# Optimization experiments

Measured on AMD Instinct MI355X. Metric: run time of the kernel, lower is better.

Reference implementation:

```python
import jax, jax.numpy as jnp
import numpy as np
import math

EPS = 1e-5  # torch LayerNorm default


def entmax15(z):
    # Peters & Martins exact sort-based alpha=1.5 entmax along last axis.
    z = z / 2.0
    z = z - jnp.max(z, axis=-1, keepdims=True)
    zs = -jnp.sort(-z, axis=-1)                      # descending
    K = z.shape[-1]
    rho = jnp.arange(1, K + 1, dtype=z.dtype)
    mean = jnp.cumsum(zs, axis=-1) / rho
    mean_sq = jnp.cumsum(zs * zs, axis=-1) / rho
    ss = rho * (mean_sq - mean * mean)
    delta = jnp.clip((1.0 - ss) / rho, 0.0)
    tau = mean - jnp.sqrt(delta)
    k = jnp.sum(tau <= zs, axis=-1, keepdims=True)   # support size
    tau_star = jnp.take_along_axis(tau, k - 1, axis=-1)
    p = jnp.square(jnp.clip(z - tau_star, 0.0))
    return p


def mish(x):
    return x * jnp.tanh(jax.nn.softplus(x))


def layer_norm(x, g, b):
    mu = jnp.mean(x, axis=-1, keepdims=True)
    var = jnp.var(x, axis=-1, keepdims=True)
    return (x - mu) / jnp.sqrt(var + EPS) * g + b


def setup_inputs() -> dict:
    key = jax.random.key(0)
    D, H, F = 512, 8, 2048
    B, S = 8, 1024
    ks = jax.random.split(key, 16)
    s = 1.0 / math.sqrt(D)
    inp = {
        "x": jax.random.normal(ks[0], (B, S, D), jnp.float32),
        # weights stored [in, out]; y = x @ W + b
        "Wq": jax.random.normal(ks[1], (D, D), jnp.float32) * s,
        "bq": jnp.zeros((D,), jnp.float32),
        "Wk": jax.random.normal(ks[2], (D, D), jnp.float32) * s,
        "bk": jnp.zeros((D,), jnp.float32),
        "Wv": jax.random.normal(ks[3], (D, D), jnp.float32) * s,
        "bv": jnp.zeros((D,), jnp.float32),
        "Wo": jax.random.normal(ks[4], (D, D), jnp.float32) * s,
        "bo": jnp.zeros((D,), jnp.float32),
        "g1": jnp.ones((D,), jnp.float32),
        "be1": jnp.zeros((D,), jnp.float32),
        "W1": jax.random.normal(ks[5], (D, F), jnp.float32) * s,
        "b1": jnp.zeros((F,), jnp.float32),
        "W2": jax.random.normal(ks[6], (F, D), jnp.float32) * (1.0 / math.sqrt(F)),
        "b2": jnp.zeros((D,), jnp.float32),
        "g2": jnp.ones((D,), jnp.float32),
        "be2": jnp.zeros((D,), jnp.float32),
    }
    return inp


def reference(x, Wq, bq, Wk, bk, Wv, bv, Wo, bo, g1, be1, W1, b1, W2, b2, g2, be2):
    B, S, D = x.shape
    H = 8
    hd = D // H
    # multi-head self-attention (z = x)
    q = (x @ Wq + bq).reshape(B, S, H, hd).transpose(0, 2, 1, 3)
    k = (x @ Wk + bk).reshape(B, S, H, hd).transpose(0, 2, 1, 3)
    v = (x @ Wv + bv).reshape(B, S, H, hd).transpose(0, 2, 1, 3)
    scores = jnp.einsum("bhqd,bhkd->bhqk", q, k) / math.sqrt(hd)
    attn = entmax15(scores)
    out = jnp.einsum("bhqk,bhkd->bhqd", attn, v)
    out = out.transpose(0, 2, 1, 3).reshape(B, S, D)
    y = out @ Wo + bo
    x = x + layer_norm(y, g1, be1)
    # feed-forward with Mish
    y = mish(x @ W1 + b1) @ W2 + b2
    x = x + layer_norm(y, g2, be2)
    return x
```

## Files before the change

### kernel.cpp

```cpp
#include <hip/hip_runtime.h>


typedef float f32x4 __attribute__((ext_vector_type(4)));
typedef float f32x2 __attribute__((ext_vector_type(2)));
typedef __bf16 b8 __attribute__((ext_vector_type(8)));

#define DEV static __device__ __forceinline__

DEV unsigned short f2bf(float f) {
  return __builtin_bit_cast(unsigned short, (__bf16)f);
}
DEV float bf2f(unsigned short b) { return __uint_as_float(((unsigned)b) << 16); }

DEV float mishf(float x) {
  if (x > 20.f) return x;
  float e = __expf(x);
  float u = 1.f + e;
  u *= u;
  return x * ((u - 1.f) / (u + 1.f));
}

DEV void async16(const void* g, void* l) {
  __builtin_amdgcn_global_load_lds(
      (const __attribute__((address_space(1))) unsigned int*)g,
      (__attribute__((address_space(3))) unsigned int*)l, 16, 0, 0);
}

DEV int mbcnt64(unsigned long long m) {
  return __builtin_amdgcn_mbcnt_hi((unsigned)(m >> 32),
                                   __builtin_amdgcn_mbcnt_lo((unsigned)m, 0));
}

template <int CTRL>
DEV float dppmov(float x) {
  return __builtin_bit_cast(
      float, __builtin_amdgcn_update_dpp(0, __builtin_bit_cast(int, x), CTRL,
                                         0xF, 0xF, true));
}
DEV float swz16(float x) {
  return __builtin_bit_cast(
      float, __builtin_amdgcn_ds_swizzle(__builtin_bit_cast(int, x), 0x401F));
}
DEV float wave_sum(float x) {
  x += dppmov<0xB1>(x);
  x += dppmov<0x4E>(x);
  x += dppmov<0x141>(x);
  x += dppmov<0x140>(x);
  x += swz16(x);
  x += __shfl_xor(x, 32);
  return x;
}
DEV float wave_max(float x) {
  x = fmaxf(x, dppmov<0xB1>(x));
  x = fmaxf(x, dppmov<0x4E>(x));
  x = fmaxf(x, dppmov<0x141>(x));
  x = fmaxf(x, dppmov<0x140>(x));
  x = fmaxf(x, swz16(x));
  x = fmaxf(x, __shfl_xor(x, 32));
  return x;
}

template <int WM, int WN, int EPI, bool OUTBF>
__global__ __launch_bounds__(256) void gemm_bt(
    const unsigned short* __restrict__ A, const unsigned short* __restrict__ Bt,
    const float* __restrict__ bias, void* __restrict__ Cp,
    int K, int lda, int ldb, int ldc,
    long sA1, long sA2, long sB1, long sB2, long sC1, long sC2,
    int hdiv, float alpha) {
  constexpr int BM = WM * 64, BN = WN * 64;
  constexpr int NA = WM * 2, NB = WN * 2;
  __shared__ unsigned short smA[BM * 64];
  __shared__ unsigned short smB[BN * 64];

  const int tid = threadIdx.x;
  const int lane = tid & 63;
  const int z = blockIdx.z;
  const long zi = z / hdiv, zr = z % hdiv;
  const unsigned short* Ab = A + zi * sA1 + zr * sA2 + (long)blockIdx.x * BM * lda;
  const unsigned short* Bb = Bt + zi * sB1 + zr * sB2 + (long)blockIdx.y * BN * ldb;

  int siA[NA];
  const unsigned short* gA[NA];
#pragma unroll
  for (int q = 0; q < NA; ++q) {
    int si = q * 256 + tid;
    int m = si >> 3, s = si & 7, g = s ^ (m & 7);
    siA[q] = si;
    gA[q] = Ab + (long)m * lda + g * 8;
  }
  int siB[NB];
  const unsigned short* gB[NB];
#pragma unroll
  for (int q = 0; q < NB; ++q) {
    int si = q * 256 + tid;
    int m = si >> 3, s = si & 7, g = s ^ (m & 7);
    siB[q] = si;
    gB[q] = Bb + (long)m * ldb + g * 8;
  }

  const int w = tid >> 6;
  const int wr = w / WN, wc = w % WN;
  const int fm = lane & 15, fg = lane >> 4;

  int aOff[4][2], bOff[4][2];
#pragma unroll
  for (int i = 0; i < 4; ++i)
#pragma unroll
    for (int ks = 0; ks < 2; ++ks) {
      int m = wr * 64 + i * 16 + fm;
      aOff[i][ks] = (m * 8 + ((ks * 4 + fg) ^ (fm & 7))) * 8;
      int n = wc * 64 + i * 16 + fm;
      bOff[i][ks] = (n * 8 + ((ks * 4 + fg) ^ (fm & 7))) * 8;
    }

  f32x4 acc[4][4];
#pragma unroll
  for (int i = 0; i < 4; ++i)
#pragma unroll
    for (int j = 0; j < 4; ++j) acc[i][j] = (f32x4){0.f, 0.f, 0.f, 0.f};

  for (int k0 = 0; k0 < K; k0 += 64) {
    __syncthreads();
#pragma unroll
    for (int q = 0; q < NA; ++q) async16(gA[q] + k0, (void*)&smA[siA[q] * 8]);
#pragma unroll
    for (int q = 0; q < NB; ++q) async16(gB[q] + k0, (void*)&smB[siB[q] * 8]);
    __syncthreads();

#pragma unroll
    for (int ks = 0; ks < 2; ++ks) {
      b8 aF[4], bF[4];
#pragma unroll
      for (int i = 0; i < 4; ++i) aF[i] = *(const b8*)&smA[aOff[i][ks]];
#pragma unroll
      for (int j = 0; j < 4; ++j) bF[j] = *(const b8*)&smB[bOff[j][ks]];
#pragma unroll
      for (int i = 0; i < 4; ++i)
#pragma unroll
        for (int j = 0; j < 4; ++j)
          acc[i][j] = __builtin_amdgcn_mfma_f32_16x16x32_bf16(aF[i], bF[j], acc[i][j], 0, 0, 0);
    }
  }

  const long cbase = zi * sC1 + zr * sC2;
  const int row0 = blockIdx.x * BM + wr * 64 + fg * 4;
  const int col0 = blockIdx.y * BN + wc * 64 + fm;
#pragma unroll
  for (int i = 0; i < 4; ++i) {
#pragma unroll
    for (int j = 0; j < 4; ++j) {
      const int col = col0 + j * 16;
      float bv = (EPI >= 1) ? bias[col] : 0.f;
#pragma unroll
      for (int r = 0; r < 4; ++r) {
        const int row = row0 + i * 16 + r;
        float v = acc[i][j][r] * alpha + bv;
        if (EPI == 2) v = mishf(v);
        const long idx = cbase + (long)row * ldc + col;
        if constexpr (OUTBF)
          ((unsigned short*)Cp)[idx] = f2bf(v);
        else
          ((float*)Cp)[idx] = v;
      }
    }
  }
}

__global__ __launch_bounds__(256) void gemm_scores(
    const unsigned short* __restrict__ QKV, unsigned short* __restrict__ P) {
  __shared__ unsigned short smB[128 * 64];

  const int tid = threadIdx.x, lane = tid & 63, w = tid >> 6;
  const int wr = w >> 1, wc = w & 1;
  const int fm = lane & 15, fg = lane >> 4;
  const int z = blockIdx.z, b = z >> 3, h = z & 7;
  const long qrow0 = (long)b * 1024 + blockIdx.x * 128;
  const long krow0 = (long)b * 1024 + blockIdx.y * 128;

#pragma unroll
  for (int q = 0; q < 4; ++q) {
    int si = q * 256 + tid;
    int m = si >> 3, s = si & 7, g = s ^ (m & 7);
    async16(QKV + (krow0 + m) * 1536 + 512 + h * 64 + g * 8, (void*)&smB[si * 8]);
  }

  b8 aQ[4][2];
#pragma unroll
  for (int i = 0; i < 4; ++i) {
    const unsigned short* qp =
        QKV + (qrow0 + wr * 64 + i * 16 + fm) * 1536 + h * 64 + fg * 8;
    aQ[i][0] = *(const b8*)qp;
    aQ[i][1] = *(const b8*)(qp + 32);
  }

  __syncthreads();

  f32x4 acc[4][4];
#pragma unroll
  for (int i = 0; i < 4; ++i)
#pragma unroll
    for (int j = 0; j < 4; ++j) acc[i][j] = (f32x4){0.f, 0.f, 0.f, 0.f};

#pragma unroll
  for (int ks = 0; ks < 2; ++ks) {
    b8 bF[4];
#pragma unroll
    for (int j = 0; j < 4; ++j) {
      int n = wc * 64 + j * 16 + fm;
      bF[j] = *(const b8*)&smB[(n * 8 + ((ks * 4 + fg) ^ (fm & 7))) * 8];
    }
#pragma unroll
    for (int i = 0; i < 4; ++i)
#pragma unroll
      for (int j = 0; j < 4; ++j)
        acc[i][j] = __builtin_amdgcn_mfma_f32_16x16x32_bf16(aQ[i][ks], bF[j], acc[i][j], 0, 0, 0);
  }

  unsigned short* Pb = P + (long)z * 1024 * 1024;
  const int row0 = blockIdx.x * 128 + wr * 64 + fg * 4;
  const int col0 = blockIdx.y * 128 + wc * 64 + fm;
#pragma unroll
  for (int i = 0; i < 4; ++i)
#pragma unroll
    for (int j = 0; j < 4; ++j)
#pragma unroll
      for (int r = 0; r < 4; ++r)
        Pb[(long)(row0 + i * 16 + r) * 1024 + col0 + j * 16] =
            f2bf(acc[i][j][r] * 0.0625f);
}

__global__ __launch_bounds__(256) void gemm_pv(
    const unsigned short* __restrict__ P, const unsigned short* __restrict__ Vt,
    const float* __restrict__ Tau, unsigned short* __restrict__ attn) {
  __shared__ unsigned short smA[256 * 64];
  __shared__ unsigned short smB[64 * 64];

  const int tid = threadIdx.x, lane = tid & 63, w = tid >> 6;
  const int fm = lane & 15, fg = lane >> 4;
  const int z = blockIdx.z;
  const long SS = 1024L * 1024L;
  const unsigned short* Ab = P + (long)z * SS + (long)blockIdx.x * 256 * 1024;
  const unsigned short* Bb = Vt + (long)z * 64 * 1024;
  const float* Tb = Tau + (long)z * 1024 + blockIdx.x * 256;

  int siA[8];
  const unsigned short* gA[8];
  float tq[8];
#pragma unroll
  for (int q = 0; q < 8; ++q) {
    int si = q * 256 + tid;
    int m = si >> 3, s = si & 7, g = s ^ (m & 7);
    siA[q] = si;
    gA[q] = Ab + (long)m * 1024 + g * 8;
    tq[q] = Tb[m];
  }
  int siB[2];
  const unsigned short* gB[2];
#pragma unroll
  for (int q = 0; q < 2; ++q) {
    int si = q * 256 + tid;
    int m = si >> 3, s = si & 7, g = s ^ (m & 7);
    siB[q] = si;
    gB[q] = Bb + (long)m * 1024 + g * 8;
  }

  int aOff[4][2], bOff[4][2];
#pragma unroll
  for (int i = 0; i < 4; ++i)
#pragma unroll
    for (int ks = 0; ks < 2; ++ks) {
      int m = w * 64 + i * 16 + fm;
      aOff[i][ks] = (m * 8 + ((ks * 4 + fg) ^ (fm & 7))) * 8;
      int n = i * 16 + fm;
      bOff[i][ks] = (n * 8 + ((ks * 4 + fg) ^ (fm & 7))) * 8;
    }

  f32x4 acc[4][4];
#pragma unroll
  for (int i = 0; i < 4; ++i)
#pragma unroll
    for (int j = 0; j < 4; ++j) acc[i][j] = (f32x4){0.f, 0.f, 0.f, 0.f};

  union AB { b8 v; unsigned short u[8]; };
  for (int k0 = 0; k0 < 1024; k0 += 64) {
    __syncthreads();
    AB areg[8];
#pragma unroll
    for (int q = 0; q < 8; ++q) areg[q].v = *(const b8*)(gA[q] + k0);
#pragma unroll
    for (int q = 0; q < 2; ++q) async16(gB[q] + k0, (void*)&smB[siB[q] * 8]);
#pragma unroll
    for (int q = 0; q < 8; ++q) {
      AB o;
#pragma unroll
      for (int e = 0; e < 8; ++e) {
        float h = fmaxf(bf2f(areg[q].u[e]) - tq[q], 0.f);
        o.u[e] = f2bf(h * h);
      }
      *(b8*)&smA[siA[q] * 8] = o.v;
    }
    __syncthreads();

#pragma unroll
    for (int ks = 0; ks < 2; ++ks) {
      b8 aF[4], bF[4];
#pragma unroll
      for (int i = 0; i < 4; ++i) aF[i] = *(const b8*)&smA[aOff[i][ks]];
#pragma unroll
      for (int j = 0; j < 4; ++j) bF[j] = *(const b8*)&smB[bOff[j][ks]];
#pragma unroll
      for (int i = 0; i < 4; ++i)
#pragma unroll
        for (int j = 0; j < 4; ++j)
          acc[i][j] = __builtin_amdgcn_mfma_f32_16x16x32_bf16(aF[i], bF[j], acc[i][j], 0, 0, 0);
    }
  }

  const long cbase = (long)(z >> 3) * 1024 * 512 + (z & 7) * 64;
  const int row0 = blockIdx.x * 256 + w * 64 + fg * 4;
#pragma unroll
  for (int i = 0; i < 4; ++i)
#pragma unroll
    for (int j = 0; j < 4; ++j) {
      const int col = fm + j * 16;
#pragma unroll
      for (int r = 0; r < 4; ++r) {
        const int row = row0 + i * 16 + r;
        attn[cbase + (long)row * 512 + col] = f2bf(acc[i][j][r]);
      }
    }
}

__global__ __launch_bounds__(256) void gemm_ffn1(
    const unsigned short* __restrict__ A, const unsigned short* __restrict__ Bt,
    const float* __restrict__ bias, unsigned short* __restrict__ C) {
  __shared__ unsigned short smA[2 * 128 * 64];
  __shared__ unsigned short smB[2 * 128 * 64];

  const int tid = threadIdx.x;
  const int lane = tid & 63;
  const unsigned short* Ab = A + (long)blockIdx.x * 128 * 512;
  const unsigned short* Bb = Bt + (long)blockIdx.y * 128 * 512;

  int siA[4], siB[4];
  const unsigned short* gA[4];
  const unsigned short* gB[4];
#pragma unroll
  for (int q = 0; q < 4; ++q) {
    int si = q * 256 + tid;
    int m = si >> 3, s = si & 7, g = s ^ (m & 7);
    siA[q] = si;
    siB[q] = si;
    gA[q] = Ab + (long)m * 512 + g * 8;
    gB[q] = Bb + (long)m * 512 + g * 8;
  }

  const int w = tid >> 6;
  const int wr = w >> 1, wc = w & 1;
  const int fm = lane & 15, fg = lane >> 4;

  int aOff[4][2], bOff[4][2];
#pragma unroll
  for (int i = 0; i < 4; ++i)
#pragma unroll
    for (int ks = 0; ks < 2; ++ks) {
      int m = wr * 64 + i * 16 + fm;
      aOff[i][ks] = (m * 8 + ((ks * 4 + fg) ^ (fm & 7))) * 8;
      int n = wc * 64 + i * 16 + fm;
      bOff[i][ks] = (n * 8 + ((ks * 4 + fg) ^ (fm & 7))) * 8;
    }

  f32x4 acc[4][4];
#pragma unroll
  for (int i = 0; i < 4; ++i)
#pragma unroll
    for (int j = 0; j < 4; ++j) acc[i][j] = (f32x4){0.f, 0.f, 0.f, 0.f};

  auto stage = [&](int buf, int k0) {
    unsigned short* dA = smA + buf * (128 * 64);
    unsigned short* dB = smB + buf * (128 * 64);
#pragma unroll
    for (int q = 0; q < 4; ++q) async16(gA[q] + k0, (void*)&dA[siA[q] * 8]);
#pragma unroll
    for (int q = 0; q < 4; ++q) async16(gB[q] + k0, (void*)&dB[siB[q] * 8]);
  };
  auto compute = [&](int buf) {
    const unsigned short* sA = smA + buf * (128 * 64);
    const unsigned short* sB = smB + buf * (128 * 64);
#pragma unroll
    for (int ks = 0; ks < 2; ++ks) {
      b8 aF[4], bF[4];
#pragma unroll
      for (int i = 0; i < 4; ++i) aF[i] = *(const b8*)&sA[aOff[i][ks]];
#pragma unroll
      for (int j = 0; j < 4; ++j) bF[j] = *(const b8*)&sB[bOff[j][ks]];
#pragma unroll
      for (int i = 0; i < 4; ++i)
#pragma unroll
        for (int j = 0; j < 4; ++j)
          acc[i][j] = __builtin_amdgcn_mfma_f32_16x16x32_bf16(aF[i], bF[j], acc[i][j], 0, 0, 0);
    }
  };

  stage(0, 0);
  __syncthreads();
  int cur = 0;
  for (int k0 = 64; k0 < 512; k0 += 64) {
    stage(cur ^ 1, k0);
    compute(cur);
    __syncthreads();
    cur ^= 1;
  }
  compute(cur);

  const int row0 = blockIdx.x * 128 + wr * 64 + fg * 4;
  const int col0 = blockIdx.y * 128 + wc * 64 + fm;
#pragma unroll
  for (int i = 0; i < 4; ++i) {
#pragma unroll
    for (int j = 0; j < 4; ++j) {
      const int col = col0 + j * 16;
      const float bv = bias[col];
#pragma unroll
      for (int r = 0; r < 4; ++r) {
        const int row = row0 + i * 16 + r;
        C[(long)row * 2048 + col] = f2bf(mishf(acc[i][j][r] + bv));
      }
    }
  }
}

template <int NC>
DEV float solve_tau(const f32x2* zc, float tau) {
  int kprev = -1;
  const f32x2 zero2 = (f32x2){0.f, 0.f};
  for (int it = 0; it < 12; ++it) {
    const f32x2 t2 = (f32x2){tau, tau};
    f32x2 s1v = zero2, s2v = zero2;
    int k = 0;
#pragma unroll
    for (int i = 0; i < NC; ++i) {
      f32x2 h = zc[i] - t2;
      k += __popcll(__ballot(h.x > 0.f));
      k += __popcll(__ballot(h.y > 0.f));
      f32x2 hp = __builtin_elementwise_max(h, zero2);
      s1v += hp;
      s2v += hp * hp;
    }
    float s1 = wave_sum(s1v.x + s1v.y);
    float s2 = wave_sum(s2v.x + s2v.y);
    if (k == kprev) break;
    kprev = k;
    float kf = (float)k;
    float disc = fmaxf(fmaf(s1, s1, -kf * (s2 - 1.f)), 0.f);
    tau += (s1 - __builtin_sqrtf(disc)) / kf;
  }
  return tau;
}

DEV float solve_tau_lds(const float* cw, int nch, int lane, float tau) {
  int kprev = -1;
  const f32x2 zero2 = (f32x2){0.f, 0.f};
  for (int it = 0; it < 12; ++it) {
    const f32x2 t2 = (f32x2){tau, tau};
    f32x2 s1v = zero2, s2v = zero2;
    int k = 0;
    for (int c = 0; c < nch; ++c) {
      f32x2 h = *(const f32x2*)&cw[c * 128 + lane * 2] - t2;
      k += __popcll(__ballot(h.x > 0.f));
      k += __popcll(__ballot(h.y > 0.f));
      f32x2 hp = __builtin_elementwise_max(h, zero2);
      s1v += hp;
      s2v += hp * hp;
    }
    float s1 = wave_sum(s1v.x + s1v.y);
    float s2 = wave_sum(s2v.x + s2v.y);
    if (k == kprev) break;
    kprev = k;
    float kf = (float)k;
    float disc = fmaxf(fmaf(s1, s1, -kf * (s2 - 1.f)), 0.f);
    tau += (s1 - __builtin_sqrtf(disc)) / kf;
  }
  return tau;
}

__global__ __launch_bounds__(256) void entmax_tau(const unsigned short* __restrict__ P,
                                                  float* __restrict__ T) {
  const int tid = threadIdx.x, lane = tid & 63, wv = tid >> 6;
  const long row = (long)blockIdx.x * 4 + wv;
  const unsigned short* p = P + row * 1024;
  __shared__ float cand[4][1024];

  union { uint4 v; unsigned short u[8]; } a, b;
  a.v = *(const uint4*)(p + lane * 16);
  b.v = *(const uint4*)(p + lane * 16 + 8);
  f32x2 zp[8];
#pragma unroll
  for (int i = 0; i < 4; ++i) {
    zp[i] = (f32x2){bf2f(a.u[2 * i]), bf2f(a.u[2 * i + 1])};
    zp[4 + i] = (f32x2){bf2f(b.u[2 * i]), bf2f(b.u[2 * i + 1])};
  }

  f32x2 mv = zp[0];
#pragma unroll
  for (int i = 1; i < 8; ++i) mv = __builtin_elementwise_max(mv, zp[i]);
  float m = wave_max(fmaxf(mv.x, mv.y));

  const float thr = m - 1.f;
  float* cw = cand[wv];

  int base = 0;
#pragma unroll
  for (int i = 0; i < 8; ++i) {
    unsigned long long mx = __ballot(zp[i].x > thr);
    if (zp[i].x > thr) cw[base + mbcnt64(mx)] = zp[i].x;
    base += __popcll(mx);
    unsigned long long my = __ballot(zp[i].y > thr);
    if (zp[i].y > thr) cw[base + mbcnt64(my)] = zp[i].y;
    base += __popcll(my);
  }

  const int nch = (base + 127) >> 7;
  for (int i = base + lane; i < nch * 128; i += 64) cw[i] = -1e30f;

  float tau;
  if (nch == 1) {
    f32x2 zc[1];
    zc[0] = *(const f32x2*)&cw[lane * 2];
    tau = solve_tau<1>(zc, thr);
  } else if (nch == 2) {
    f32x2 zc[2];
    zc[0] = *(const f32x2*)&cw[lane * 2];
    zc[1] = *(const f32x2*)&cw[128 + lane * 2];
    tau = solve_tau<2>(zc, thr);
  } else {
    tau = solve_tau_lds(cw, nch, lane, thr);
  }

  if (lane == 0) T[row] = tau;
}

__global__ __launch_bounds__(256) void prep_all(
    const float* __restrict__ x, unsigned short* __restrict__ xb,
    const float* __restrict__ Wq, const float* __restrict__ Wk,
    const float* __restrict__ Wv, const float* __restrict__ Wo,
    const float* __restrict__ W1, const float* __restrict__ W2,
    unsigned short* __restrict__ Wqkvt, unsigned short* __restrict__ Wot,
    unsigned short* __restrict__ W1t, unsigned short* __restrict__ W2t,
    const float* __restrict__ bq, const float* __restrict__ bk,
    const float* __restrict__ bv, float* __restrict__ bqkv) {
  __shared__ float t[32][33];
  const int bid = blockIdx.x, tid = threadIdx.x;

  if (bid < 4096) {
    long i = ((long)bid * 256 + tid) * 4;
    float4 v = *(const float4*)&x[i];
    uint2 pk;
    pk.x = (unsigned)f2bf(v.x) | ((unsigned)f2bf(v.y) << 16);
    pk.y = (unsigned)f2bf(v.z) | ((unsigned)f2bf(v.w) << 16);
    *(uint2*)&xb[i] = pk;
    return;
  }

  const float* in;
  unsigned short* out;
  int ldi, ldo, bx, by;
  if (bid < 5120) {
    int t4 = (bid - 4096) >> 8, local = (bid - 4096) & 255;
    const float* ins[4] = {Wq, Wk, Wv, Wo};
    unsigned short* outs[4] = {Wqkvt, Wqkvt + 512 * 512, Wqkvt + 2 * 512 * 512, Wot};
    in = ins[t4];
    out = outs[t4];
    ldi = 512;
    ldo = 512;
    bx = local & 15;
    by = local >> 4;
  } else if (bid < 6144) {
    int local = bid - 5120;
    in = W1;
    out = W1t;
    ldi = 2048;
    ldo = 512;
    bx = local & 63;
    by = local >> 6;
  } else if (bid < 7168) {
    int local = bid - 6144;
    in = W2;
    out = W2t;
    ldi = 512;
    ldo = 2048;
    bx = local & 15;
    by = local >> 4;
  } else {
    int i = (bid - 7168) * 256 + tid;
    if (i < 512) bqkv[i] = bq[i];
    else if (i < 1024) bqkv[i] = bk[i - 512];
    else if (i < 1536) bqkv[i] = bv[i - 1024];
    return;
  }

  const int tx = tid & 31, ty = tid >> 5;
  const int r0 = by * 32, c0 = bx * 32;
#pragma unroll
  for (int q = 0; q < 4; ++q) {
    int r = ty + q * 8;
    t[r][tx] = in[(long)(r0 + r) * ldi + c0 + tx];
  }
  __syncthreads();
#pragma unroll
  for (int q = 0; q < 4; ++q) {
    int r = ty + q * 8;
    out[(long)(c0 + r) * ldo + r0 + tx] = f2bf(t[tx][r]);
  }
}

__global__ __launch_bounds__(256) void transpose_b2b(const unsigned short* __restrict__ in,
                                                     unsigned short* __restrict__ out,
                                                     int ldi, int ldo, long i1, long i2,
                                                     long o1, long o2, int hdiv) {
  __shared__ unsigned short t[32][33];
  const int z = blockIdx.z;
  in += (long)(z / hdiv) * i1 + (long)(z % hdiv) * i2;
  out += (long)(z / hdiv) * o1 + (long)(z % hdiv) * o2;
  const int tx = threadIdx.x & 31, ty = threadIdx.x >> 5;
  const int r0 = blockIdx.y * 32, c0 = blockIdx.x * 32;
#pragma unroll
  for (int q = 0; q < 4; ++q) {
    int r = ty + q * 8;
    t[r][tx] = in[(long)(r0 + r) * ldi + c0 + tx];
  }
  __syncthreads();
#pragma unroll
  for (int q = 0; q < 4; ++q) {
    int r = ty + q * 8;
    out[(long)(c0 + r) * ldo + r0 + tx] = t[tx][r];
  }
}

template <bool WB, int NS>
__global__ __launch_bounds__(256) void ln_res(const float* __restrict__ xin,
                                              const float* __restrict__ y, long ystr,
                                              const float* __restrict__ ybias,
                                              const float* __restrict__ g,
                                              const float* __restrict__ be,
                                              float* __restrict__ xo,
                                              unsigned short* __restrict__ xob) {
  const int row = blockIdx.x, tid = threadIdx.x, lane = tid & 63, wv = tid >> 6;
  const long base = (long)row * 512 + tid * 2;
  const int c = tid * 2;
  float2 v = *(const float2*)&y[base];
#pragma unroll
  for (int j = 1; j < NS; ++j) {
    float2 u = *(const float2*)&y[base + j * ystr];
    v.x += u.x;
    v.y += u.y;
  }
  v.x += ybias[c];
  v.y += ybias[c + 1];
  float s1 = wave_sum(v.x + v.y);
  float s2 = wave_sum(v.x * v.x + v.y * v.y);
  __shared__ float red[4][2];
  if (lane == 0) {
    red[wv][0] = s1;
    red[wv][1] = s2;
  }
  __syncthreads();
  s1 = red[0][0] + red[1][0] + red[2][0] + red[3][0];
  s2 = red[0][1] + red[1][1] + red[2][1] + red[3][1];
  const float mu = s1 * (1.f / 512.f);
  const float rstd = rsqrtf(s2 * (1.f / 512.f) - mu * mu + 1e-5f);
  float2 xv = *(const float2*)&xin[base];
  float o0 = xv.x + (v.x - mu) * rstd * g[c] + be[c];
  float o1 = xv.y + (v.y - mu) * rstd * g[c + 1] + be[c + 1];
  float2 ov;
  ov.x = o0;
  ov.y = o1;
  *(float2*)&xo[base] = ov;
  if constexpr (WB) {
    unsigned pk = (unsigned)f2bf(o0) | ((unsigned)f2bf(o1) << 16);
    *(unsigned*)&xob[base] = pk;
  }
}

extern "C" void kernel_launch(void* const* d_in, const int* in_sizes, int n_in,
                              void* d_out, int out_size, void* d_ws, size_t ws_size,
                              hipStream_t stream) {
  const int B = 8, S = 1024, D = 512, H = 8, F = 2048;
  const int BS = B * S;
  const int N3 = 3 * D;

  const float* x = (const float*)d_in[0];
  const float* Wq = (const float*)d_in[1];
  const float* bq = (const float*)d_in[2];
  const float* Wk = (const float*)d_in[3];
  const float* bk = (const float*)d_in[4];
  const float* Wv = (const float*)d_in[5];
  const float* bv = (const float*)d_in[6];
  const float* Wo = (const float*)d_in[7];
  const float* bo = (const float*)d_in[8];
  const float* g1 = (const float*)d_in[9];
  const float* be1 = (const float*)d_in[10];
  const float* W1 = (const float*)d_in[11];
  const float* b1 = (const float*)d_in[12];
  const float* W2 = (const float*)d_in[13];
  const float* b2 = (const float*)d_in[14];
  const float* g2 = (const float*)d_in[15];
  const float* be2 = (const float*)d_in[16];
  float* out = (float*)d_out;

  char* w = (char*)d_ws;
  size_t off = 0;
  auto alloc = [&](size_t bytes) -> void* {
    void* p = w + off;
    off += bytes;
    off = (off + 255) & ~(size_t)255;
    return p;
  };

  unsigned short* xb = (unsigned short*)alloc((size_t)BS * D * 2);
  unsigned short* Wqkvt = (unsigned short*)alloc((size_t)N3 * D * 2);
  unsigned short* Wot = (unsigned short*)alloc((size_t)D * D * 2);
  unsigned short* W1t = (unsigned short*)alloc((size_t)F * D * 2);
  unsigned short* W2t = (unsigned short*)alloc((size_t)D * F * 2);
  float* bqkv = (float*)alloc((size_t)N3 * 4);
  unsigned short* QKVb = (unsigned short*)alloc((size_t)BS * N3 * 2);
  unsigned short* Vt = (unsigned short*)alloc((size_t)BS * D * 2);
  unsigned short* attn = (unsigned short*)alloc((size_t)BS * D * 2);
  unsigned short* P = (unsigned short*)alloc((size_t)B * H * S * S * 2);
  float* Tau = (float*)alloc((size_t)B * H * S * 4);
  float* x1 = (float*)alloc((size_t)BS * D * 4);
  unsigned short* hb = (unsigned short*)alloc((size_t)BS * F * 2);
  unsigned short* x1b = xb;
  float* yp = (float*)P;
  const long PSTR = (long)BS * D;

  prep_all<<<7174, 256, 0, stream>>>(x, xb, Wq, Wk, Wv, Wo, W1, W2,
                                     Wqkvt, Wot, W1t, W2t, bq, bk, bv, bqkv);

  gemm_bt<2, 2, 1, true><<<dim3(BS / 128, N3 / 128, 1), 256, 0, stream>>>(
      xb, Wqkvt, bqkv, QKVb, D, D, D, N3, 0, 0, 0, 0, 0, 0, 1, 1.f);

  transpose_b2b<<<dim3(2, 32, 64), 256, 0, stream>>>(
      QKVb + 1024, Vt, N3, S, (long)S * N3, 64, (long)8 * 64 * S, (long)64 * S, 8);

  gemm_scores<<<dim3(S / 128, S / 128, B * H), 256, 0, stream>>>(QKVb, P);

  entmax_tau<<<(B * H * S) / 4, 256, 0, stream>>>(P, Tau);

  gemm_pv<<<dim3(S / 256, 1, B * H), 256, 0, stream>>>(P, Vt, Tau, attn);

  gemm_bt<2, 2, 0, false><<<dim3(BS / 128, D / 128, 2), 256, 0, stream>>>(
      attn, Wot, nullptr, yp, D / 2, D, D, D, 0, D / 2, 0, D / 2, 0, PSTR, 2, 1.f);

  ln_res<true, 2><<<BS, 256, 0, stream>>>(x, yp, PSTR, bo, g1, be1, x1, x1b);

  gemm_ffn1<<<dim3(BS / 128, F / 128, 1), 256, 0, stream>>>(x1b, W1t, b1, hb);

  gemm_bt<2, 2, 0, false><<<dim3(BS / 128, D / 128, 2), 256, 0, stream>>>(
      hb, W2t, nullptr, yp, F / 2, F, F, D, 0, F / 2, 0, F / 2, 0, PSTR, 2, 1.f);

  ln_res<false, 2><<<BS, 256, 0, stream>>>(x1, yp, PSTR, b2, g2, be2, out, nullptr);
}
```

Measured before the change: 342.4 us.

## Apply entmax in place and use async-loaded 128-row PV GEMM

The entmax kernel now computes the final probabilities and writes them back over the scores buffer instead of storing only tau. The PV GEMM then loads P straight to LDS with async global-to-LDS copies and no per-element transform, using 128-row tiles to double the grid. This removes the transform from the GEMM's load path and improves occupancy, at the cost of an extra full write of the large probability matrix.

```diff
diff --git a/kernel.cpp b/kernel.cpp
--- a/kernel.cpp
+++ b/kernel.cpp
@@ -229,30 +229,27 @@
             f2bf(acc[i][j][r] * 0.0625f);
 }
 
-__global__ __launch_bounds__(256) void gemm_pv(
+__global__ __launch_bounds__(256) void gemm_pv128(
     const unsigned short* __restrict__ P, const unsigned short* __restrict__ Vt,
-    const float* __restrict__ Tau, unsigned short* __restrict__ attn) {
-  __shared__ unsigned short smA[256 * 64];
+    unsigned short* __restrict__ attn) {
+  __shared__ unsigned short smA[128 * 64];
   __shared__ unsigned short smB[64 * 64];
 
   const int tid = threadIdx.x, lane = tid & 63, w = tid >> 6;
   const int fm = lane & 15, fg = lane >> 4;
   const int z = blockIdx.z;
   const long SS = 1024L * 1024L;
-  const unsigned short* Ab = P + (long)z * SS + (long)blockIdx.x * 256 * 1024;
+  const unsigned short* Ab = P + (long)z * SS + (long)blockIdx.x * 128 * 1024;
   const unsigned short* Bb = Vt + (long)z * 64 * 1024;
-  const float* Tb = Tau + (long)z * 1024 + blockIdx.x * 256;
-
-  int siA[8];
-  const unsigned short* gA[8];
-  float tq[8];
-#pragma unroll
-  for (int q = 0; q < 8; ++q) {
+
+  int siA[4];
+  const unsigned short* gA[4];
+#pragma unroll
+  for (int q = 0; q < 4; ++q) {
     int si = q * 256 + tid;
     int m = si >> 3, s = si & 7, g = s ^ (m & 7);
     siA[q] = si;
     gA[q] = Ab + (long)m * 1024 + g * 8;
-    tq[q] = Tb[m];
   }
   int siB[2];
   const unsigned short* gB[2];
@@ -264,52 +261,44 @@
     gB[q] = Bb + (long)m * 1024 + g * 8;
   }
 
-  int aOff[4][2], bOff[4][2];
-#pragma unroll
-  for (int i = 0; i < 4; ++i)
-#pragma unroll
-    for (int ks = 0; ks < 2; ++ks) {
-      int m = w * 64 + i * 16 + fm;
+  int aOff[2][2], bOff[4][2];
+#pragma unroll
+  for (int ks = 0; ks < 2; ++ks) {
+#pragma unroll
+    for (int i = 0; i < 2; ++i) {
+      int m = w * 32 + i * 16 + fm;
       aOff[i][ks] = (m * 8 + ((ks * 4 + fg) ^ (fm & 7))) * 8;
-      int n = i * 16 + fm;
-      bOff[i][ks] = (n * 8 + ((ks * 4 + fg) ^ (fm & 7))) * 8;
-    }
-
-  f32x4 acc[4][4];
-#pragma unroll
-  for (int i = 0; i < 4; ++i)
+    }
+#pragma unroll
+    for (int j = 0; j < 4; ++j) {
+      int n = j * 16 + fm;
+      bOff[j][ks] = (n * 8 + ((ks * 4 + fg) ^ (fm & 7))) * 8;
+    }
+  }
+
+  f32x4 acc[2][4];
+#pragma unroll
+  for (int i = 0; i < 2; ++i)
 #pragma unroll
     for (int j = 0; j < 4; ++j) acc[i][j] = (f32x4){0.f, 0.f, 0.f, 0.f};
 
-  union AB { b8 v; unsigned short u[8]; };
   for (int k0 = 0; k0 < 1024; k0 += 64) {
     __syncthreads();
-    AB areg[8];
-#pragma unroll
-    for (int q = 0; q < 8; ++q) areg[q].v = *(const b8*)(gA[q] + k0);
+#pragma unroll
+    for (int q = 0; q < 4; ++q) async16(gA[q] + k0, (void*)&smA[siA[q] * 8]);
 #pragma unroll
     for (int q = 0; q < 2; ++q) async16(gB[q] + k0, (void*)&smB[siB[q] * 8]);
-#pragma unroll
-    for (int q = 0; q < 8; ++q) {
-      AB o;
-#pragma unroll
-      for (int e = 0; e < 8; ++e) {
-        float h = fmaxf(bf2f(areg[q].u[e]) - tq[q], 0.f);
-        o.u[e] = f2bf(h * h);
-      }
-      *(b8*)&smA[siA[q] * 8] = o.v;
-    }
     __syncthreads();
 
 #pragma unroll
     for (int ks = 0; ks < 2; ++ks) {
-      b8 aF[4], bF[4];
-#pragma unroll
-      for (int i = 0; i < 4; ++i) aF[i] = *(const b8*)&smA[aOff[i][ks]];
+      b8 aF[2], bF[4];
+#pragma unroll
+      for (int i = 0; i < 2; ++i) aF[i] = *(const b8*)&smA[aOff[i][ks]];
 #pragma unroll
       for (int j = 0; j < 4; ++j) bF[j] = *(const b8*)&smB[bOff[j][ks]];
 #pragma unroll
-      for (int i = 0; i < 4; ++i)
+      for (int i = 0; i < 2; ++i)
 #pragma unroll
         for (int j = 0; j < 4; ++j)
           acc[i][j] = __builtin_amdgcn_mfma_f32_16x16x32_bf16(aF[i], bF[j], acc[i][j], 0, 0, 0);
@@ -317,9 +306,9 @@
   }
 
   const long cbase = (long)(z >> 3) * 1024 * 512 + (z & 7) * 64;
-  const int row0 = blockIdx.x * 256 + w * 64 + fg * 4;
-#pragma unroll
-  for (int i = 0; i < 4; ++i)
+  const int row0 = blockIdx.x * 128 + w * 32 + fg * 4;
+#pragma unroll
+  for (int i = 0; i < 2; ++i)
 #pragma unroll
     for (int j = 0; j < 4; ++j) {
       const int col = fm + j * 16;
@@ -484,11 +473,10 @@
   return tau;
 }
 
-__global__ __launch_bounds__(256) void entmax_tau(const unsigned short* __restrict__ P,
-                                                  float* __restrict__ T) {
+__global__ __launch_bounds__(256) void entmax_rows(unsigned short* __restrict__ P) {
   const int tid = threadIdx.x, lane = tid & 63, wv = tid >> 6;
   const long row = (long)blockIdx.x * 4 + wv;
-  const unsigned short* p = P + row * 1024;
+  unsigned short* p = P + row * 1024;
   __shared__ float cand[4][1024];
 
   union { uint4 v; unsigned short u[8]; } a, b;
@@ -537,7 +525,20 @@
     tau = solve_tau_lds(cw, nch, lane, thr);
   }
 
-  if (lane == 0) T[row] = tau;
+  const f32x2 t2 = (f32x2){tau, tau};
+  const f32x2 zero2 = (f32x2){0.f, 0.f};
+#pragma unroll
+  for (int i = 0; i < 4; ++i) {
+    f32x2 h0 = __builtin_elementwise_max(zp[i] - t2, zero2);
+    f32x2 h1 = __builtin_elementwise_max(zp[4 + i] - t2, zero2);
+    f32x2 p0 = h0 * h0, p1 = h1 * h1;
+    a.u[2 * i] = f2bf(p0.x);
+    a.u[2 * i + 1] = f2bf(p0.y);
+    b.u[2 * i] = f2bf(p1.x);
+    b.u[2 * i + 1] = f2bf(p1.y);
+  }
+  *(uint4*)(p + lane * 16) = a.v;
+  *(uint4*)(p + lane * 16 + 8) = b.v;
 }
 
 __global__ __launch_bounds__(256) void prep_all(
@@ -727,7 +728,6 @@
   unsigned short* Vt = (unsigned short*)alloc((size_t)BS * D * 2);
   unsigned short* attn = (unsigned short*)alloc((size_t)BS * D * 2);
   unsigned short* P = (unsigned short*)alloc((size_t)B * H * S * S * 2);
-  float* Tau = (float*)alloc((size_t)B * H * S * 4);
   float* x1 = (float*)alloc((size_t)BS * D * 4);
   unsigned short* hb = (unsigned short*)alloc((size_t)BS * F * 2);
   unsigned short* x1b = xb;
@@ -745,9 +745,9 @@
 
   gemm_scores<<<dim3(S / 128, S / 128, B * H), 256, 0, stream>>>(QKVb, P);
 
-  entmax_tau<<<(B * H * S) / 4, 256, 0, stream>>>(P, Tau);
-
-  gemm_pv<<<dim3(S / 256, 1, B * H), 256, 0, stream>>>(P, Vt, Tau, attn);
+  entmax_rows<<<(B * H * S) / 4, 256, 0, stream>>>(P);
+
+  gemm_pv128<<<dim3(S / 128, 1, B * H), 256, 0, stream>>>(P, Vt, attn);
 
   gemm_bt<2, 2, 0, false><<<dim3(BS / 128, D / 128, 2), 256, 0, stream>>>(
       attn, Wot, nullptr, yp, D / 2, D, D, D, 0, D / 2, 0, D / 2, 0, PSTR, 2, 1.f);
```

Measured after the change: 337.1 us. No clear change (-1.5%).
